# Kernel optimization log

Hardware: AMD Instinct MI355X
Metric: run time of the kernel (lower is better)

The kernel has to match this reference:

```python
import jax, jax.numpy as jnp
import numpy as np

B, L, F, DM, H, DFF, NL, PRED = 8, 1000, 7, 512, 8, 2048, 4, 50
DK = DM // H           # head dim 64
P = DK // 4            # learned-mask proj dim 16
EPS = 1e-5
SCALE = 1.0 / float(np.sqrt(DK))


def _ln(x, g, b):
    m = jnp.mean(x, -1, keepdims=True)
    v = jnp.mean((x - m) ** 2, -1, keepdims=True)
    return (x - m) / jnp.sqrt(v + EPS) * g + b


def _make_pe():
    pos = np.arange(L, dtype=np.float32)[:, None]
    div = np.exp(np.arange(0, DM, 2, dtype=np.float32) * (-np.log(10000.0) / DM))
    pe = np.zeros((L, DM), dtype=np.float32)
    pe[:, 0::2] = np.sin(pos * div)
    pe[:, 1::2] = np.cos(pos * div)
    return jnp.asarray(pe)


def setup_inputs() -> dict:
    key = jax.random.key(0)
    ks = iter(jax.random.split(key, 40))
    def w(shape, s=0.02):
        return jax.random.normal(next(ks), shape, jnp.float32) * s
    return {
        "x": jax.random.normal(next(ks), (B, L, F), jnp.float32),
        "emb_w": w((F, DM)), "emb_b": jnp.zeros((DM,), jnp.float32),
        "pe": _make_pe(),
        "Wq": w((NL, DM, DM)), "bq": jnp.zeros((NL, DM), jnp.float32),
        "Wk": w((NL, DM, DM)), "bk": jnp.zeros((NL, DM), jnp.float32),
        "Wv": w((NL, DM, DM)), "bv": jnp.zeros((NL, DM), jnp.float32),
        "Wo": w((NL, DM, DM)), "bo": jnp.zeros((NL, DM), jnp.float32),
        "W1": w((NL, DM, DFF)), "b1": jnp.zeros((NL, DFF), jnp.float32),
        "W2": w((NL, DFF, DM)), "b2": jnp.zeros((NL, DM), jnp.float32),
        "g1": jnp.ones((NL, DM), jnp.float32), "be1": jnp.zeros((NL, DM), jnp.float32),
        "g2": jnp.ones((NL, DM), jnp.float32), "be2": jnp.zeros((NL, DM), jnp.float32),
        "lm_qw": w((DK, P)), "lm_qb": jnp.zeros((P,), jnp.float32),
        "lm_kw": w((DK, P)), "lm_kb": jnp.zeros((P,), jnp.float32),
        "gn": jnp.ones((DM,), jnp.float32), "bn": jnp.zeros((DM,), jnp.float32),
        "fc_w": w((DM, PRED)), "fc_b": jnp.zeros((PRED,), jnp.float32),
    }


def reference(x, emb_w, emb_b, pe, Wq, bq, Wk, bk, Wv, bv, Wo, bo,
              W1, b1, W2, b2, g1, be1, g2, be2,
              lm_qw, lm_qb, lm_kw, lm_kb, gn, bn, fc_w, fc_b):
    # eval mode: dropout = identity
    h = x @ emb_w + emb_b + pe[None]                 # [B,L,DM]
    for i in range(NL):
        q = (h @ Wq[i] + bq[i]).reshape(B, L, H, DK)
        k = (h @ Wk[i] + bk[i]).reshape(B, L, H, DK)
        v = (h @ Wv[i] + bv[i]).reshape(B, L, H, DK)
        scores = jnp.einsum('blhd,bshd->bhls', q, k) * SCALE
        # shared LearnedMask: per-head Q/K projection to P dims, tanh bias
        qp = q @ lm_qw + lm_qb                       # [B,L,H,P]
        kp = k @ lm_kw + lm_kb                       # [B,S,H,P]
        scores = scores + jnp.tanh(jnp.einsum('blhp,bshp->bhls', qp, kp))
        attn = jax.nn.softmax(scores, axis=-1)       # mask_flag=False: no mask
        ctx = jnp.einsum('bhls,bshd->blhd', attn, v).reshape(B, L, DM)
        h = _ln(h + ctx @ Wo[i] + bo[i], g1[i], be1[i])
        y = jax.nn.relu(h @ W1[i] + b1[i]) @ W2[i] + b2[i]
        h2 = _ln(h + y, g2[i], be2[i])
        h = _ln(h2 + y, g2[i], be2[i])               # module applies norm2 twice
    h = _ln(h, gn, bn)                               # Encoder final norm
    return h[:, -1, :] @ fc_w + fc_b                 # [B, PRED]
```

## Files before the change

### kernel.cpp

```cpp
#include <hip/hip_runtime.h>
#include <math.h>

#define B_    8
#define L_    1000
#define F_    7
#define DM_   512
#define H_    8
#define DFF_  2048
#define NL_   4
#define PRED_ 50
#define DK_   64
#define P_    16
#define EPS_  1e-5f
#define QKVS  1536

#define L2E_   1.4426950408889634f
#define C_QS   0.18033688011112042f
#define WS_QP  16.0f
#define BS_QP  2.8853900817779268f
#define SHFT_  24.0f

typedef unsigned short u16;
typedef __bf16 bf16x8 __attribute__((ext_vector_type(8)));
typedef float  f32x4  __attribute__((ext_vector_type(4)));

__device__ inline float wave_reduce_sum(float x) {
#pragma unroll
  for (int off = 32; off >= 1; off >>= 1) x += __shfl_xor(x, off, 64);
  return x;
}
__device__ inline u16 f2bf(float f) {
  unsigned int u = __float_as_uint(f);
  unsigned int r = u + 0x7FFFu + ((u >> 16) & 1u);
  return (u16)(r >> 16);
}
__device__ inline float bf2f(u16 u) { return __uint_as_float(((unsigned int)u) << 16); }
__device__ inline float fexp2(float x) { return __builtin_amdgcn_exp2f(x); }
__device__ inline float frcp(float x) { return __builtin_amdgcn_rcpf(x); }

union bfrag { bf16x8 b; uint4 q; u16 u[8]; };

__device__ inline void gload16(const u16* g, u16* l) {
  __builtin_amdgcn_global_load_lds(
      (const __attribute__((address_space(1))) void*)g,
      (__attribute__((address_space(3))) void*)l, 16, 0, 0);
}

__global__ __launch_bounds__(256)
void transpose_w(const float* __restrict__ in, u16* __restrict__ out,
                 int K, int N, size_t in_lstride, size_t out_lstride,
                 int row_off, int out_ld) {
  __shared__ float tile[32][33];
  int z = blockIdx.z;
  int kk0 = blockIdx.y * 32, nn0 = blockIdx.x * 32;
  int tx = threadIdx.x & 31, ty = threadIdx.x >> 5;
  const float* ip = in + z * in_lstride;
  u16* op = out + z * out_lstride;
#pragma unroll
  for (int i = 0; i < 4; i++)
    tile[ty + i * 8][tx] = ip[(size_t)(kk0 + ty + i * 8) * N + nn0 + tx];
  __syncthreads();
#pragma unroll
  for (int i = 0; i < 4; i++)
    op[(size_t)(row_off + nn0 + ty + i * 8) * out_ld + kk0 + tx] = f2bf(tile[tx][ty + i * 8]);
}

__global__ __launch_bounds__(256)
void vtrans_kernel(const u16* __restrict__ qkv, u16* __restrict__ vtg) {
  __shared__ u16 tile[32][33];
  int bh = blockIdx.z;
  int b = bh >> 3, hh = bh & 7;
  int k0 = blockIdx.x * 32;
  int d0 = blockIdx.y * 32;
  int tx = threadIdx.x & 31, ty = threadIdx.x >> 5;
#pragma unroll
  for (int i = 0; i < 4; i++) {
    int key = k0 + ty + i * 8;
    u16 v = 0;
    if (key < L_) v = qkv[(size_t)(b * L_ + key) * QKVS + 1024 + hh * DK_ + d0 + tx];
    tile[ty + i * 8][tx] = v;
  }
  __syncthreads();
#pragma unroll
  for (int i = 0; i < 4; i++)
    vtg[((size_t)bh * DK_ + d0 + ty + i * 8) * 1024 + k0 + tx] = tile[tx][ty + i * 8];
}

__global__ __launch_bounds__(256)
void concat_bias(const float* __restrict__ bq, const float* __restrict__ bk,
                 const float* __restrict__ bv, float* __restrict__ bqkv) {
  int i = blockIdx.x * 256 + threadIdx.x;
  int l = i / QKVS, j = i % QKVS;
  float v = (j < 512) ? bq[l * 512 + j] : (j < 1024) ? bk[l * 512 + j - 512]
                                                     : bv[l * 512 + j - 1024];
  bqkv[i] = v;
}

__global__ __launch_bounds__(512)
void embed_kernel(const float* __restrict__ x, const float* __restrict__ emb_w,
                  const float* __restrict__ emb_b, const float* __restrict__ pe,
                  float* __restrict__ h, u16* __restrict__ h16) {
  int bl = blockIdx.x;
  int l = bl % L_;
  int d = threadIdx.x;
  const float* xr = x + (size_t)bl * F_;
  float acc = emb_b[d] + pe[(size_t)l * DM_ + d];
#pragma unroll
  for (int f = 0; f < F_; f++) acc = fmaf(xr[f], emb_w[f * DM_ + d], acc);
  h[(size_t)bl * DM_ + d] = acc;
  h16[(size_t)bl * DM_ + d] = f2bf(acc);
}

template<int BN>
__global__ __launch_bounds__(256)
void gemm16(const u16* __restrict__ A, const u16* __restrict__ Bt,
            const float* __restrict__ bias, const float* __restrict__ resid,
            float* __restrict__ C32, u16* __restrict__ C16,
            int M, int K, int N, int relu, int nscale, float sval) {
  constexpr int NTW = BN / 32;
  constexpr int BG  = BN / 32;
  __shared__ u16 As[128 * 64];
  __shared__ u16 Bs[BN * 64];
  int t = threadIdx.x;
  int w = t >> 6, lane = t & 63;
  int wr = w >> 1, wc = w & 1;
  int mloc = lane & 15, quad = lane >> 4;
  int m0 = blockIdx.y * 128, n0 = blockIdx.x * BN;

  const u16* agp[4]; u16* alds[4];
#pragma unroll
  for (int j = 0; j < 4; j++) {
    int r = w * 32 + j * 8 + (lane >> 3);
    int gm = m0 + r; if (gm > M - 1) gm = M - 1;
    int ch = (lane & 7) ^ (r & 7);
    agp[j] = A + (size_t)gm * K + ch * 8;
    alds[j] = As + (w * 32 + j * 8) * 64;
  }
  const u16* bgp[BG]; u16* blds[BG];
#pragma unroll
  for (int j = 0; j < BG; j++) {
    int r = w * (8 * BG) + j * 8 + (lane >> 3);
    int ch = (lane & 7) ^ (r & 7);
    bgp[j] = Bt + (size_t)(n0 + r) * K + ch * 8;
    blds[j] = Bs + (w * (8 * BG) + j * 8) * 64;
  }
  const u16* apt[2][4];
#pragma unroll
  for (int mi = 0; mi < 4; mi++) {
    int tr = wr * 64 + mi * 16 + mloc;
    apt[0][mi] = As + tr * 64 + ((quad ^ (tr & 7)) * 8);
    apt[1][mi] = As + tr * 64 + (((4 + quad) ^ (tr & 7)) * 8);
  }
  const u16* bpt[2][NTW];
#pragma unroll
  for (int nt = 0; nt < NTW; nt++) {
    int tr = wc * (BN / 2) + nt * 16 + mloc;
    bpt[0][nt] = Bs + tr * 64 + ((quad ^ (tr & 7)) * 8);
    bpt[1][nt] = Bs + tr * 64 + (((4 + quad) ^ (tr & 7)) * 8);
  }

  f32x4 acc[4][NTW];
#pragma unroll
  for (int mi = 0; mi < 4; mi++)
#pragma unroll
    for (int nt = 0; nt < NTW; nt++) acc[mi][nt] = (f32x4){0.f, 0.f, 0.f, 0.f};

  for (int k0 = 0; k0 < K; k0 += 64) {
    __syncthreads();
    #pragma unroll
    for (int j = 0; j < 4; j++) gload16(agp[j] + k0, alds[j]);
    #pragma unroll
    for (int j = 0; j < BG; j++) gload16(bgp[j] + k0, blds[j]);
    __syncthreads();
#pragma unroll
    for (int kc = 0; kc < 2; kc++) {
      bf16x8 af[4], bv[NTW];
#pragma unroll
      for (int mi = 0; mi < 4; mi++) af[mi] = *(const bf16x8*)apt[kc][mi];
#pragma unroll
      for (int nt = 0; nt < NTW; nt++) bv[nt] = *(const bf16x8*)bpt[kc][nt];
#pragma unroll
      for (int mi = 0; mi < 4; mi++)
#pragma unroll
        for (int nt = 0; nt < NTW; nt++)
          acc[mi][nt] = __builtin_amdgcn_mfma_f32_16x16x32_bf16(af[mi], bv[nt], acc[mi][nt], 0, 0, 0);
    }
  }

#pragma unroll
  for (int mi = 0; mi < 4; mi++) {
#pragma unroll
    for (int r = 0; r < 4; r++) {
      int m = m0 + wr * 64 + mi * 16 + quad * 4 + r;
      if (m >= M) continue;
      size_t crow = (size_t)m * N;
#pragma unroll
      for (int nt = 0; nt < NTW; nt++) {
        int n = n0 + wc * (BN / 2) + nt * 16 + mloc;
        float vsum = acc[mi][nt][r] + bias[n];
        if (resid) vsum += resid[crow + n];
        if (n < nscale) vsum *= sval;
        if (relu) vsum = fmaxf(vsum, 0.f);
        if (C32) C32[crow + n] = vsum;
        if (C16) C16[crow + n] = f2bf(vsum);
      }
    }
  }
}

__global__ __launch_bounds__(128)
void lmproj_kernel(const u16* __restrict__ qkv,
                   const float* __restrict__ wq, const float* __restrict__ bq,
                   const float* __restrict__ wk, const float* __restrict__ bk,
                   u16* __restrict__ qp, u16* __restrict__ kp) {
  int bl = blockIdx.x;
  int which = blockIdx.y;
  int t = threadIdx.x;
  int hh = t >> 4, p = t & 15;
  const float* w  = which ? wk : wq;
  const float* bb = which ? bk : bq;
  u16* dst        = which ? kp : qp;
  float wscale = which ? 1.0f : WS_QP;
  float bscale = which ? 1.0f : BS_QP;
  const u16* s = qkv + (size_t)bl * QKVS + (which ? 512 : 0) + hh * DK_;
  float acc = 0.f;
#pragma unroll
  for (int d = 0; d < DK_; d++) acc = fmaf(bf2f(s[d]), w[d * P_ + p], acc);
  dst[((size_t)bl * H_ + hh) * P_ + p] = f2bf(fmaf(acc, wscale, bb[p] * bscale));
}

#define KT   128
#define LDP  136
#define KPLD 24
__global__ __launch_bounds__(256)
void attn_mfma_kernel(const u16* __restrict__ qkv, const u16* __restrict__ qpg,
                      const u16* __restrict__ kpg, const u16* __restrict__ vtg,
                      u16* __restrict__ ctx) {
  __shared__ u16 KsPs[4 * 16 * LDP];
  __shared__ u16 Vt[64 * KT];
  __shared__ u16 Kp[KT * KPLD];

  int Lid = blockIdx.x;
  int qt = Lid >> 6;
  int bh = ((Lid & 7) << 3) | ((Lid >> 3) & 7);
  int b = bh >> 3, hh = bh & 7;
  int l0 = qt * 64;
  int t = threadIdx.x;
  int wv = t >> 6, lane = t & 63;
  int m = lane & 15, quad = lane >> 4;

  int lq = l0 + wv * 16 + m; if (lq > L_ - 1) lq = L_ - 1;
  const u16* qrow = qkv + (size_t)(b * L_ + lq) * QKVS + hh * DK_;
  bf16x8 qa0 = *(const bf16x8*)(qrow + quad * 8);
  bf16x8 qa1 = *(const bf16x8*)(qrow + 32 + quad * 8);
  bfrag qpa;
  if (quad < 2) {
    qpa.q = *(const uint4*)(qpg + ((size_t)(b * L_ + lq) * H_ + hh) * P_ + quad * 8);
  } else {
    qpa.q = make_uint4(0u, 0u, 0u, 0u);
  }

  const u16* ks_g = qkv + ((size_t)b * L_ + (t >> 3)) * QKVS + 512 + hh * DK_
                    + ((t & 7) ^ ((t >> 3) & 7)) * 8;
  u16* ks_l = KsPs + (t >> 6) * 512;
  const u16* vt_g = vtg + ((size_t)bh * DK_ + (t >> 4)) * 1024
                    + (((t & 15) ^ (t >> 4)) * 8);
  u16* vt_l = Vt + (t >> 6) * 512;

  f32x4 O[4];
#pragma unroll
  for (int nt = 0; nt < 4; nt++) O[nt] = (f32x4){0.f, 0.f, 0.f, 0.f};
  float lrun[4] = {0.f, 0.f, 0.f, 0.f};

  u16* pw = KsPs + wv * (16 * LDP);
  const u16* pr0 = pw + m * LDP + quad * 8;

  for (int s0 = 0; s0 < L_; s0 += KT) {
    uint4 p0, p1;
    if (t < KT) {
      int sg2 = s0 + t; if (sg2 > L_ - 1) sg2 = L_ - 1;
      const u16* pr = kpg + ((size_t)(b * L_ + sg2) * H_ + hh) * P_;
      p0 = *(const uint4*)(pr);
      p1 = *(const uint4*)(pr + 8);
    }
    __syncthreads();
#pragma unroll
    for (int j = 0; j < 4; j++) {
      gload16(ks_g + ((size_t)s0 + j * 32) * QKVS, ks_l + j * 2048);
      gload16(vt_g + s0 + (size_t)j * 16 * 1024, vt_l + j * 2048);
    }
    if (t < KT) {
      *(uint4*)&Kp[t * KPLD]     = p0;
      *(uint4*)&Kp[t * KPLD + 8] = p1;
    }
    __syncthreads();

    float scp[8][4];
    const f32x4 zz = (f32x4){0.f, 0.f, 0.f, 0.f};
#pragma unroll
    for (int nt = 0; nt < 8; nt++) {
      const u16* kb = KsPs + (nt * 16 + m) * 64;
      int x0 = ((quad) ^ (m & 7)) * 8;
      int x1 = ((4 + quad) ^ (m & 7)) * 8;
      f32x4 sacc = __builtin_amdgcn_mfma_f32_16x16x32_bf16(qa0, *(const bf16x8*)(kb + x0), zz, 0, 0, 0);
      sacc = __builtin_amdgcn_mfma_f32_16x16x32_bf16(qa1, *(const bf16x8*)(kb + x1), sacc, 0, 0, 0);
      bf16x8 kpf = *(const bf16x8*)(Kp + (nt * 16 + m) * KPLD + (quad & 1) * 8);
      f32x4 macc = __builtin_amdgcn_mfma_f32_16x16x32_bf16(qpa.b, kpf, zz, 0, 0, 0);
#pragma unroll
      for (int r = 0; r < 4; r++) {
        float e = fexp2(macc[r]);
        float d = frcp(e + 1.f);
        float th = fmaf(d, -2.f * L2E_, L2E_);
        scp[nt][r] = sacc[r] + th;
      }
    }
    if (s0 + KT > L_) {
#pragma unroll
      for (int nt = 0; nt < 8; nt++) {
        if (s0 + nt * 16 + m >= L_) {
#pragma unroll
          for (int r = 0; r < 4; r++) scp[nt][r] = -3e38f;
        }
      }
    }
#pragma unroll
    for (int nt = 0; nt < 8; nt++)
#pragma unroll
      for (int r = 0; r < 4; r++) {
        float p = fexp2(scp[nt][r] - SHFT_);
        scp[nt][r] = p;
        lrun[r] += p;
      }

    __syncthreads();

#pragma unroll
    for (int nt = 0; nt < 8; nt++)
#pragma unroll
      for (int r = 0; r < 4; r++)
        pw[(quad * 4 + r) * LDP + nt * 16 + m] = f2bf(scp[nt][r]);

#pragma unroll
    for (int kc = 0; kc < 4; kc++) {
      bf16x8 pa = *(const bf16x8*)(pr0 + kc * 32);
#pragma unroll
      for (int nt = 0; nt < 4; nt++) {
        const u16* vb = Vt + (nt * 16 + m) * KT + (((kc * 4 + quad) ^ m) * 8);
        O[nt] = __builtin_amdgcn_mfma_f32_16x16x32_bf16(pa, *(const bf16x8*)vb, O[nt], 0, 0, 0);
      }
    }
  }

  float inv[4];
#pragma unroll
  for (int r = 0; r < 4; r++) {
#pragma unroll
    for (int msk = 1; msk < 16; msk <<= 1) lrun[r] += __shfl_xor(lrun[r], msk, 64);
    inv[r] = frcp(lrun[r]);
  }
#pragma unroll
  for (int r = 0; r < 4; r++) {
    int l = l0 + wv * 16 + quad * 4 + r;
    if (l >= L_) continue;
    u16* crow = ctx + ((size_t)(b * L_ + l)) * DM_ + hh * DK_;
#pragma unroll
    for (int nt = 0; nt < 4; nt++) crow[nt * 16 + m] = f2bf(O[nt][r] * inv[r]);
  }
}

__global__ __launch_bounds__(256)
void ln_kernel(const float* __restrict__ a, const float* __restrict__ badd,
               const float* __restrict__ g, const float* __restrict__ be,
               float* __restrict__ o, u16* __restrict__ o16) {
  int row = blockIdx.x;
  int t = threadIdx.x;
  size_t base = (size_t)row * DM_;
  float x0 = a[base + t], x1 = a[base + t + 256];
  if (badd) { x0 += badd[base + t]; x1 += badd[base + t + 256]; }
  float s = wave_reduce_sum(x0 + x1);
  float ss = wave_reduce_sum(x0 * x0 + x1 * x1);
  __shared__ float sh_s[4], sh_ss[4];
  int wv = t >> 6, lane = t & 63;
  if (lane == 0) { sh_s[wv] = s; sh_ss[wv] = ss; }
  __syncthreads();
  float S = sh_s[0] + sh_s[1] + sh_s[2] + sh_s[3];
  float SS = sh_ss[0] + sh_ss[1] + sh_ss[2] + sh_ss[3];
  float mean = S * (1.0f / DM_);
  float var = SS * (1.0f / DM_) - mean * mean;
  float rstd = rsqrtf(var + EPS_);
  float r0 = (x0 - mean) * rstd * g[t] + be[t];
  float r1 = (x1 - mean) * rstd * g[t + 256] + be[t + 256];
  o[base + t] = r0; o[base + t + 256] = r1;
  if (o16) { o16[base + t] = f2bf(r0); o16[base + t + 256] = f2bf(r1); }
}

__global__ __launch_bounds__(256)
void ln2x_kernel(const float* __restrict__ hin, const float* __restrict__ y,
                 const float* __restrict__ g, const float* __restrict__ be,
                 float* __restrict__ o32, u16* __restrict__ o16) {
  int row = blockIdx.x;
  int t = threadIdx.x;
  size_t base = (size_t)row * DM_;
  float y0 = y[base + t], y1 = y[base + t + 256];
  float x0 = hin[base + t] + y0, x1 = hin[base + t + 256] + y1;
  __shared__ float sh_s[4], sh_ss[4];
  int wv = t >> 6, lane = t & 63;
  float g0 = g[t], g1v = g[t + 256], b0 = be[t], b1v = be[t + 256];

  float s = wave_reduce_sum(x0 + x1);
  float ss = wave_reduce_sum(x0 * x0 + x1 * x1);
  if (lane == 0) { sh_s[wv] = s; sh_ss[wv] = ss; }
  __syncthreads();
  float S = sh_s[0] + sh_s[1] + sh_s[2] + sh_s[3];
  float SS = sh_ss[0] + sh_ss[1] + sh_ss[2] + sh_ss[3];
  float mean = S * (1.0f / DM_);
  float var = SS * (1.0f / DM_) - mean * mean;
  float rstd = rsqrtf(var + EPS_);
  float h20 = (x0 - mean) * rstd * g0 + b0 + y0;
  float h21 = (x1 - mean) * rstd * g1v + b1v + y1;
  __syncthreads();

  s = wave_reduce_sum(h20 + h21);
  ss = wave_reduce_sum(h20 * h20 + h21 * h21);
  if (lane == 0) { sh_s[wv] = s; sh_ss[wv] = ss; }
  __syncthreads();
  S = sh_s[0] + sh_s[1] + sh_s[2] + sh_s[3];
  SS = sh_ss[0] + sh_ss[1] + sh_ss[2] + sh_ss[3];
  mean = S * (1.0f / DM_);
  var = SS * (1.0f / DM_) - mean * mean;
  rstd = rsqrtf(var + EPS_);
  float r0 = (h20 - mean) * rstd * g0 + b0;
  float r1 = (h21 - mean) * rstd * g1v + b1v;
  o32[base + t] = r0; o32[base + t + 256] = r1;
  if (o16) { o16[base + t] = f2bf(r0); o16[base + t + 256] = f2bf(r1); }
}

__global__ __launch_bounds__(512)
void final_kernel(const float* __restrict__ h, const float* __restrict__ gn,
                  const float* __restrict__ bn, const float* __restrict__ fcw,
                  const float* __restrict__ fcb, float* __restrict__ out) {
  int b = blockIdx.x;
  int t = threadIdx.x;
  size_t base = ((size_t)b * L_ + (L_ - 1)) * DM_;
  float x = h[base + t];
  float s = wave_reduce_sum(x);
  float ss = wave_reduce_sum(x * x);
  __shared__ float sh_s[8], sh_ss[8];
  int wv = t >> 6, lane = t & 63;
  if (lane == 0) { sh_s[wv] = s; sh_ss[wv] = ss; }
  __syncthreads();
  float S = 0.f, SS = 0.f;
#pragma unroll
  for (int i = 0; i < 8; i++) { S += sh_s[i]; SS += sh_ss[i]; }
  float mean = S * (1.0f / DM_);
  float var = SS * (1.0f / DM_) - mean * mean;
  float rstd = rsqrtf(var + EPS_);
  __shared__ float hn[DM_];
  hn[t] = (x - mean) * rstd * gn[t] + bn[t];
  __syncthreads();
  if (t < PRED_) {
    float acc = fcb[t];
#pragma unroll 8
    for (int d = 0; d < DM_; d++) acc = fmaf(hn[d], fcw[d * PRED_ + t], acc);
    out[b * PRED_ + t] = acc;
  }
}

extern "C" void kernel_launch(void* const* d_in, const int* in_sizes, int n_in,
                              void* d_out, int out_size, void* d_ws, size_t ws_size,
                              hipStream_t stream) {
  const float* x     = (const float*)d_in[0];
  const float* emb_w = (const float*)d_in[1];
  const float* emb_b = (const float*)d_in[2];
  const float* pe    = (const float*)d_in[3];
  const float* Wq = (const float*)d_in[4];  const float* bq = (const float*)d_in[5];
  const float* Wk = (const float*)d_in[6];  const float* bk = (const float*)d_in[7];
  const float* Wv = (const float*)d_in[8];  const float* bv = (const float*)d_in[9];
  const float* Wo = (const float*)d_in[10]; const float* bo = (const float*)d_in[11];
  const float* W1 = (const float*)d_in[12]; const float* b1 = (const float*)d_in[13];
  const float* W2 = (const float*)d_in[14]; const float* b2 = (const float*)d_in[15];
  const float* g1 = (const float*)d_in[16]; const float* be1 = (const float*)d_in[17];
  const float* g2 = (const float*)d_in[18]; const float* be2 = (const float*)d_in[19];
  const float* lm_qw = (const float*)d_in[20]; const float* lm_qb = (const float*)d_in[21];
  const float* lm_kw = (const float*)d_in[22]; const float* lm_kb = (const float*)d_in[23];
  const float* gn = (const float*)d_in[24]; const float* bn = (const float*)d_in[25];
  const float* fc_w = (const float*)d_in[26]; const float* fc_b = (const float*)d_in[27];
  float* out = (float*)d_out;

  const size_t ROWS = (size_t)B_ * L_;
  u16* qkv16 = (u16*)d_ws;
  u16* ctx16 = qkv16 + ROWS * QKVS;
  u16* ffn1  = qkv16;
  u16* h16   = ctx16 + ROWS * DM_;
  u16* qp16  = h16 + ROWS * DM_;
  u16* kp16  = qp16 + ROWS * H_ * P_;
  u16* Wqkv_t = kp16 + ROWS * H_ * P_;
  u16* Wo_t   = Wqkv_t + (size_t)NL_ * QKVS * DM_;
  u16* W1_t   = Wo_t + (size_t)NL_ * DM_ * DM_;
  u16* W2_t   = W1_t + (size_t)NL_ * DFF_ * DM_;
  float* h32  = (float*)(W2_t + (size_t)NL_ * DM_ * DFF_);
  float* t0   = h32 + ROWS * DM_;
  float* bqkv = t0 + ROWS * DM_;
  u16* vtg    = (u16*)t0;

  transpose_w<<<dim3(16, 16, NL_), 256, 0, stream>>>(Wq, Wqkv_t, DM_, DM_, (size_t)DM_ * DM_, (size_t)QKVS * DM_, 0, DM_);
  transpose_w<<<dim3(16, 16, NL_), 256, 0, stream>>>(Wk, Wqkv_t, DM_, DM_, (size_t)DM_ * DM_, (size_t)QKVS * DM_, 512, DM_);
  transpose_w<<<dim3(16, 16, NL_), 256, 0, stream>>>(Wv, Wqkv_t, DM_, DM_, (size_t)DM_ * DM_, (size_t)QKVS * DM_, 1024, DM_);
  transpose_w<<<dim3(16, 16, NL_), 256, 0, stream>>>(Wo, Wo_t, DM_, DM_, (size_t)DM_ * DM_, (size_t)DM_ * DM_, 0, DM_);
  transpose_w<<<dim3(64, 16, NL_), 256, 0, stream>>>(W1, W1_t, DM_, DFF_, (size_t)DM_ * DFF_, (size_t)DFF_ * DM_, 0, DM_);
  transpose_w<<<dim3(16, 64, NL_), 256, 0, stream>>>(W2, W2_t, DFF_, DM_, (size_t)DFF_ * DM_, (size_t)DM_ * DFF_, 0, DFF_);
  concat_bias<<<NL_ * QKVS / 256, 256, 0, stream>>>(bq, bk, bv, bqkv);

  embed_kernel<<<dim3((unsigned)ROWS), 512, 0, stream>>>(x, emb_w, emb_b, pe, h32, h16);

  dim3 g_qkv(QKVS / 128, 63);
  dim3 g_ffn1(DFF_ / 128, 63);
  dim3 g_n512(DM_ / 64, 63);
  dim3 g_attn(1024);
  dim3 g_lm((unsigned)ROWS, 2);

  for (int i = 0; i < NL_; i++) {
    gemm16<128><<<g_qkv, 256, 0, stream>>>(h16, Wqkv_t + (size_t)i * QKVS * DM_,
        bqkv + i * QKVS, nullptr, nullptr, qkv16, 8000, DM_, QKVS, 0, 512, C_QS);

    lmproj_kernel<<<g_lm, 128, 0, stream>>>(qkv16, lm_qw, lm_qb, lm_kw, lm_kb, qp16, kp16);
    vtrans_kernel<<<dim3(32, 2, B_ * H_), 256, 0, stream>>>(qkv16, vtg);

    attn_mfma_kernel<<<g_attn, 256, 0, stream>>>(qkv16, qp16, kp16, vtg, ctx16);

    gemm16<64><<<g_n512, 256, 0, stream>>>(ctx16, Wo_t + (size_t)i * DM_ * DM_,
        bo + i * DM_, h32, t0, nullptr, 8000, DM_, DM_, 0, 0, 1.0f);
    ln_kernel<<<dim3((unsigned)ROWS), 256, 0, stream>>>(t0, nullptr, g1 + i * DM_, be1 + i * DM_, h32, h16);

    gemm16<128><<<g_ffn1, 256, 0, stream>>>(h16, W1_t + (size_t)i * DFF_ * DM_,
        b1 + i * DFF_, nullptr, nullptr, ffn1, 8000, DM_, DFF_, 1, 0, 1.0f);
    gemm16<64><<<g_n512, 256, 0, stream>>>(ffn1, W2_t + (size_t)i * DM_ * DFF_,
        b2 + i * DM_, nullptr, t0, nullptr, 8000, DFF_, DM_, 0, 0, 1.0f);

    ln2x_kernel<<<dim3((unsigned)ROWS), 256, 0, stream>>>(h32, t0, g2 + i * DM_, be2 + i * DM_, h32, h16);
  }

  final_kernel<<<B_, 512, 0, stream>>>(h32, gn, bn, fc_w, fc_b, out);
}
```

Baseline: 1.260 ms.

## Fold learned-mask projections into QKV GEMM and write transposed V from epilogue

Precomputes fused weights (Wq·lm_qw, Wk·lm_kw) and biases so the QKV GEMM also emits the 16-dim mask projections as extra output columns (N grows from 1536 to 1792). This removes the separate lmproj kernel. The GEMM epilogue also writes V straight into the transposed per-head layout, replacing vtrans_kernel with a small kernel that only zeroes the padding. The attention kernel is reworked to compute scores and P chunk by chunk, with a smaller P buffer, which removes a barrier and the large score register array. In exchange the GEMM does more work, and the mask projection now sees different bf16 rounding because it is applied to weights rather than to bf16 Q/K.

```diff
diff --git a/kernel.cpp b/kernel.cpp
--- a/kernel.cpp
+++ b/kernel.cpp
@@ -12,11 +12,10 @@
 #define DK_   64
 #define P_    16
 #define EPS_  1e-5f
-#define QKVS  1536
+#define QKVS  1792
 
 #define L2E_   1.4426950408889634f
 #define C_QS   0.18033688011112042f
-#define WS_QP  16.0f
 #define BS_QP  2.8853900817779268f
 #define SHFT_  24.0f
 
@@ -66,33 +65,63 @@
 }
 
 __global__ __launch_bounds__(256)
-void vtrans_kernel(const u16* __restrict__ qkv, u16* __restrict__ vtg) {
-  __shared__ u16 tile[32][33];
-  int bh = blockIdx.z;
-  int b = bh >> 3, hh = bh & 7;
-  int k0 = blockIdx.x * 32;
-  int d0 = blockIdx.y * 32;
-  int tx = threadIdx.x & 31, ty = threadIdx.x >> 5;
-#pragma unroll
-  for (int i = 0; i < 4; i++) {
-    int key = k0 + ty + i * 8;
-    u16 v = 0;
-    if (key < L_) v = qkv[(size_t)(b * L_ + key) * QKVS + 1024 + hh * DK_ + d0 + tx];
-    tile[ty + i * 8][tx] = v;
-  }
-  __syncthreads();
-#pragma unroll
-  for (int i = 0; i < 4; i++)
-    vtg[((size_t)bh * DK_ + d0 + ty + i * 8) * 1024 + k0 + tx] = tile[tx][ty + i * 8];
+void wfuse_kernel(const float* __restrict__ Wq, const float* __restrict__ Wk,
+                  const float* __restrict__ lmqw, const float* __restrict__ lmkw,
+                  u16* __restrict__ Wt) {
+  int hh = blockIdx.x, side = blockIdx.y, layer = blockIdx.z;
+  const float* W = (side ? Wk : Wq) + (size_t)layer * 512 * 512;
+  const float* lw = side ? lmkw : lmqw;
+  float scale = side ? 1.0f : BS_QP;
+  __shared__ float lws[64][17];
+  int t = threadIdx.x;
+  for (int i = t; i < 1024; i += 256) lws[i >> 4][i & 15] = lw[i];
+  __syncthreads();
+  int p = t & 15, kk = t >> 4;
+  u16* orow = Wt + (size_t)layer * QKVS * 512 + (size_t)(1536 + side * 128 + hh * 16 + p) * 512;
+  for (int kb = 0; kb < 32; kb++) {
+    int k = kb * 16 + kk;
+    const float* wr = W + (size_t)k * 512 + hh * 64;
+    float acc = 0.f;
+#pragma unroll
+    for (int d = 0; d < 64; d++) acc = fmaf(wr[d], lws[d][p], acc);
+    orow[k] = f2bf(acc * scale);
+  }
+}
+
+__global__ __launch_bounds__(192)
+void vzero_kernel(u16* __restrict__ vtg) {
+  int bh = blockIdx.x;
+  int t = threadIdx.x;
+  int dk = t / 3, c = t - dk * 3;
+  *(uint4*)(vtg + ((size_t)bh * 64 + dk) * 1024 + 1000 + c * 8) =
+      make_uint4(0u, 0u, 0u, 0u);
 }
 
 __global__ __launch_bounds__(256)
 void concat_bias(const float* __restrict__ bq, const float* __restrict__ bk,
-                 const float* __restrict__ bv, float* __restrict__ bqkv) {
+                 const float* __restrict__ bv,
+                 const float* __restrict__ lmqw, const float* __restrict__ lmqb,
+                 const float* __restrict__ lmkw, const float* __restrict__ lmkb,
+                 float* __restrict__ bqkv) {
   int i = blockIdx.x * 256 + threadIdx.x;
   int l = i / QKVS, j = i % QKVS;
-  float v = (j < 512) ? bq[l * 512 + j] : (j < 1024) ? bk[l * 512 + j - 512]
-                                                     : bv[l * 512 + j - 1024];
+  float v;
+  if (j < 512) v = bq[l * 512 + j];
+  else if (j < 1024) v = bk[l * 512 + j - 512];
+  else if (j < 1536) v = bv[l * 512 + j - 1024];
+  else if (j < 1664) {
+    int hh = (j - 1536) >> 4, p = (j - 1536) & 15;
+    float acc = lmqb[p];
+#pragma unroll
+    for (int d = 0; d < 64; d++) acc = fmaf(bq[l * 512 + hh * 64 + d], lmqw[d * 16 + p], acc);
+    v = acc * BS_QP;
+  } else {
+    int hh = (j - 1664) >> 4, p = (j - 1664) & 15;
+    float acc = lmkb[p];
+#pragma unroll
+    for (int d = 0; d < 64; d++) acc = fmaf(bk[l * 512 + hh * 64 + d], lmkw[d * 16 + p], acc);
+    v = acc;
+  }
   bqkv[i] = v;
 }
 
@@ -115,7 +144,7 @@
 __global__ __launch_bounds__(256)
 void gemm16(const u16* __restrict__ A, const u16* __restrict__ Bt,
             const float* __restrict__ bias, const float* __restrict__ resid,
-            float* __restrict__ C32, u16* __restrict__ C16,
+            float* __restrict__ C32, u16* __restrict__ C16, u16* __restrict__ vtg,
             int M, int K, int N, int relu, int nscale, float sval) {
   constexpr int NTW = BN / 32;
   constexpr int BG  = BN / 32;
@@ -167,9 +196,9 @@
 
   for (int k0 = 0; k0 < K; k0 += 64) {
     __syncthreads();
-    #pragma unroll
+#pragma unroll
     for (int j = 0; j < 4; j++) gload16(agp[j] + k0, alds[j]);
-    #pragma unroll
+#pragma unroll
     for (int j = 0; j < BG; j++) gload16(bgp[j] + k0, blds[j]);
     __syncthreads();
 #pragma unroll
@@ -189,56 +218,52 @@
 
 #pragma unroll
   for (int mi = 0; mi < 4; mi++) {
-#pragma unroll
-    for (int r = 0; r < 4; r++) {
-      int m = m0 + wr * 64 + mi * 16 + quad * 4 + r;
-      if (m >= M) continue;
-      size_t crow = (size_t)m * N;
-#pragma unroll
-      for (int nt = 0; nt < NTW; nt++) {
-        int n = n0 + wc * (BN / 2) + nt * 16 + mloc;
-        float vsum = acc[mi][nt][r] + bias[n];
-        if (resid) vsum += resid[crow + n];
-        if (n < nscale) vsum *= sval;
-        if (relu) vsum = fmaxf(vsum, 0.f);
-        if (C32) C32[crow + n] = vsum;
-        if (C16) C16[crow + n] = f2bf(vsum);
+    int m_r0 = m0 + wr * 64 + mi * 16 + quad * 4;
+#pragma unroll
+    for (int nt = 0; nt < NTW; nt++) {
+      int nbase = n0 + wc * (BN / 2) + nt * 16;
+      int n = nbase + mloc;
+      if (vtg && nbase >= 1024 && nbase < 1536) {
+        if (m_r0 < M) {
+          int bb = (m_r0 * 67109) >> 26;
+          int ll = m_r0 - bb * 1000;
+          int hh2 = (n - 1024) >> 6, dk = n & 63;
+          float bn_ = bias[n];
+          union { uint2 d; u16 s[4]; } pk;
+#pragma unroll
+          for (int r = 0; r < 4; r++) pk.s[r] = f2bf(acc[mi][nt][r] + bn_);
+          u16* dst = vtg + ((size_t)(bb * 8 + hh2) * 64 + dk) * 1024 + ll;
+          *(uint2*)dst = pk.d;
+        }
+      } else {
+        float bn_ = bias[n];
+#pragma unroll
+        for (int r = 0; r < 4; r++) {
+          int m = m_r0 + r;
+          if (m >= M) continue;
+          size_t crow = (size_t)m * N;
+          float vsum = acc[mi][nt][r] + bn_;
+          if (resid) vsum += resid[crow + n];
+          if (n < nscale) vsum *= sval;
+          if (relu) vsum = fmaxf(vsum, 0.f);
+          if (C32) C32[crow + n] = vsum;
+          if (C16) C16[crow + n] = f2bf(vsum);
+        }
       }
     }
   }
 }
 
-__global__ __launch_bounds__(128)
-void lmproj_kernel(const u16* __restrict__ qkv,
-                   const float* __restrict__ wq, const float* __restrict__ bq,
-                   const float* __restrict__ wk, const float* __restrict__ bk,
-                   u16* __restrict__ qp, u16* __restrict__ kp) {
-  int bl = blockIdx.x;
-  int which = blockIdx.y;
-  int t = threadIdx.x;
-  int hh = t >> 4, p = t & 15;
-  const float* w  = which ? wk : wq;
-  const float* bb = which ? bk : bq;
-  u16* dst        = which ? kp : qp;
-  float wscale = which ? 1.0f : WS_QP;
-  float bscale = which ? 1.0f : BS_QP;
-  const u16* s = qkv + (size_t)bl * QKVS + (which ? 512 : 0) + hh * DK_;
-  float acc = 0.f;
-#pragma unroll
-  for (int d = 0; d < DK_; d++) acc = fmaf(bf2f(s[d]), w[d * P_ + p], acc);
-  dst[((size_t)bl * H_ + hh) * P_ + p] = f2bf(fmaf(acc, wscale, bb[p] * bscale));
-}
-
 #define KT   128
-#define LDP  136
 #define KPLD 24
-__global__ __launch_bounds__(256)
-void attn_mfma_kernel(const u16* __restrict__ qkv, const u16* __restrict__ qpg,
-                      const u16* __restrict__ kpg, const u16* __restrict__ vtg,
+#define PSLD 40
+__global__ __launch_bounds__(256)
+void attn_mfma_kernel(const u16* __restrict__ qkv, const u16* __restrict__ vtg,
                       u16* __restrict__ ctx) {
-  __shared__ u16 KsPs[4 * 16 * LDP];
+  __shared__ u16 Ks[KT * 64];
   __shared__ u16 Vt[64 * KT];
   __shared__ u16 Kp[KT * KPLD];
+  __shared__ u16 Ps[4 * 16 * PSLD];
 
   int Lid = blockIdx.x;
   int qt = Lid >> 6;
@@ -255,14 +280,14 @@
   bf16x8 qa1 = *(const bf16x8*)(qrow + 32 + quad * 8);
   bfrag qpa;
   if (quad < 2) {
-    qpa.q = *(const uint4*)(qpg + ((size_t)(b * L_ + lq) * H_ + hh) * P_ + quad * 8);
+    qpa.q = *(const uint4*)(qkv + (size_t)(b * L_ + lq) * QKVS + 1536 + hh * P_ + quad * 8);
   } else {
     qpa.q = make_uint4(0u, 0u, 0u, 0u);
   }
 
   const u16* ks_g = qkv + ((size_t)b * L_ + (t >> 3)) * QKVS + 512 + hh * DK_
                     + ((t & 7) ^ ((t >> 3) & 7)) * 8;
-  u16* ks_l = KsPs + (t >> 6) * 512;
+  u16* ks_l = Ks + (t >> 6) * 512;
   const u16* vt_g = vtg + ((size_t)bh * DK_ + (t >> 4)) * 1024
                     + (((t & 15) ^ (t >> 4)) * 8);
   u16* vt_l = Vt + (t >> 6) * 512;
@@ -272,14 +297,15 @@
   for (int nt = 0; nt < 4; nt++) O[nt] = (f32x4){0.f, 0.f, 0.f, 0.f};
   float lrun[4] = {0.f, 0.f, 0.f, 0.f};
 
-  u16* pw = KsPs + wv * (16 * LDP);
-  const u16* pr0 = pw + m * LDP + quad * 8;
+  u16* pw = Ps + wv * (16 * PSLD);
+  const u16* pr0 = pw + m * PSLD + quad * 8;
+  const f32x4 zz = (f32x4){0.f, 0.f, 0.f, 0.f};
 
   for (int s0 = 0; s0 < L_; s0 += KT) {
     uint4 p0, p1;
     if (t < KT) {
       int sg2 = s0 + t; if (sg2 > L_ - 1) sg2 = L_ - 1;
-      const u16* pr = kpg + ((size_t)(b * L_ + sg2) * H_ + hh) * P_;
+      const u16* pr = qkv + (size_t)(b * L_ + sg2) * QKVS + 1664 + hh * P_;
       p0 = *(const uint4*)(pr);
       p1 = *(const uint4*)(pr + 8);
     }
@@ -295,58 +321,42 @@
     }
     __syncthreads();
 
-    float scp[8][4];
-    const f32x4 zz = (f32x4){0.f, 0.f, 0.f, 0.f};
-#pragma unroll
-    for (int nt = 0; nt < 8; nt++) {
-      const u16* kb = KsPs + (nt * 16 + m) * 64;
-      int x0 = ((quad) ^ (m & 7)) * 8;
-      int x1 = ((4 + quad) ^ (m & 7)) * 8;
-      f32x4 sacc = __builtin_amdgcn_mfma_f32_16x16x32_bf16(qa0, *(const bf16x8*)(kb + x0), zz, 0, 0, 0);
-      sacc = __builtin_amdgcn_mfma_f32_16x16x32_bf16(qa1, *(const bf16x8*)(kb + x1), sacc, 0, 0, 0);
-      bf16x8 kpf = *(const bf16x8*)(Kp + (nt * 16 + m) * KPLD + (quad & 1) * 8);
-      f32x4 macc = __builtin_amdgcn_mfma_f32_16x16x32_bf16(qpa.b, kpf, zz, 0, 0, 0);
-#pragma unroll
-      for (int r = 0; r < 4; r++) {
-        float e = fexp2(macc[r]);
-        float d = frcp(e + 1.f);
-        float th = fmaf(d, -2.f * L2E_, L2E_);
-        scp[nt][r] = sacc[r] + th;
-      }
-    }
-    if (s0 + KT > L_) {
-#pragma unroll
-      for (int nt = 0; nt < 8; nt++) {
-        if (s0 + nt * 16 + m >= L_) {
-#pragma unroll
-          for (int r = 0; r < 4; r++) scp[nt][r] = -3e38f;
+#pragma unroll
+    for (int kc = 0; kc < 4; kc++) {
+      float pv2[2][4];
+#pragma unroll
+      for (int h2 = 0; h2 < 2; h2++) {
+        int nt = kc * 2 + h2;
+        const u16* kb = Ks + (nt * 16 + m) * 64;
+        int x0 = ((quad) ^ (m & 7)) * 8;
+        int x1 = ((4 + quad) ^ (m & 7)) * 8;
+        f32x4 sacc = __builtin_amdgcn_mfma_f32_16x16x32_bf16(qa0, *(const bf16x8*)(kb + x0), zz, 0, 0, 0);
+        sacc = __builtin_amdgcn_mfma_f32_16x16x32_bf16(qa1, *(const bf16x8*)(kb + x1), sacc, 0, 0, 0);
+        bf16x8 kpf = *(const bf16x8*)(Kp + (nt * 16 + m) * KPLD + (quad & 1) * 8);
+        f32x4 macc = __builtin_amdgcn_mfma_f32_16x16x32_bf16(qpa.b, kpf, zz, 0, 0, 0);
+        bool oob = (s0 + nt * 16 + m) >= L_;
+#pragma unroll
+        for (int r = 0; r < 4; r++) {
+          float e = fexp2(macc[r]);
+          float d = frcp(e + 1.f);
+          float th = fmaf(d, -2.f * L2E_, L2E_);
+          float s = sacc[r] + th;
+          if (oob) s = -3e38f;
+          float p = fexp2(s - SHFT_);
+          pv2[h2][r] = p;
+          lrun[r] += p;
         }
       }
-    }
-#pragma unroll
-    for (int nt = 0; nt < 8; nt++)
-#pragma unroll
-      for (int r = 0; r < 4; r++) {
-        float p = fexp2(scp[nt][r] - SHFT_);
-        scp[nt][r] = p;
-        lrun[r] += p;
-      }
-
-    __syncthreads();
-
-#pragma unroll
-    for (int nt = 0; nt < 8; nt++)
-#pragma unroll
-      for (int r = 0; r < 4; r++)
-        pw[(quad * 4 + r) * LDP + nt * 16 + m] = f2bf(scp[nt][r]);
-
-#pragma unroll
-    for (int kc = 0; kc < 4; kc++) {
-      bf16x8 pa = *(const bf16x8*)(pr0 + kc * 32);
-#pragma unroll
-      for (int nt = 0; nt < 4; nt++) {
-        const u16* vb = Vt + (nt * 16 + m) * KT + (((kc * 4 + quad) ^ m) * 8);
-        O[nt] = __builtin_amdgcn_mfma_f32_16x16x32_bf16(pa, *(const bf16x8*)vb, O[nt], 0, 0, 0);
+#pragma unroll
+      for (int h2 = 0; h2 < 2; h2++)
+#pragma unroll
+        for (int r = 0; r < 4; r++)
+          pw[(quad * 4 + r) * PSLD + h2 * 16 + m] = f2bf(pv2[h2][r]);
+      bf16x8 pa = *(const bf16x8*)pr0;
+#pragma unroll
+      for (int ntd = 0; ntd < 4; ntd++) {
+        const u16* vb = Vt + (ntd * 16 + m) * KT + (((kc * 4 + quad) ^ m) * 8);
+        O[ntd] = __builtin_amdgcn_mfma_f32_16x16x32_bf16(pa, *(const bf16x8*)vb, O[ntd], 0, 0, 0);
       }
     }
   }
@@ -492,9 +502,7 @@
   u16* ctx16 = qkv16 + ROWS * QKVS;
   u16* ffn1  = qkv16;
   u16* h16   = ctx16 + ROWS * DM_;
-  u16* qp16  = h16 + ROWS * DM_;
-  u16* kp16  = qp16 + ROWS * H_ * P_;
-  u16* Wqkv_t = kp16 + ROWS * H_ * P_;
+  u16* Wqkv_t = h16 + ROWS * DM_;
   u16* Wo_t   = Wqkv_t + (size_t)NL_ * QKVS * DM_;
   u16* W1_t   = Wo_t + (size_t)NL_ * DM_ * DM_;
   u16* W2_t   = W1_t + (size_t)NL_ * DFF_ * DM_;
@@ -509,7 +517,8 @@
   transpose_w<<<dim3(16, 16, NL_), 256, 0, stream>>>(Wo, Wo_t, DM_, DM_, (size_t)DM_ * DM_, (size_t)DM_ * DM_, 0, DM_);
   transpose_w<<<dim3(64, 16, NL_), 256, 0, stream>>>(W1, W1_t, DM_, DFF_, (size_t)DM_ * DFF_, (size_t)DFF_ * DM_, 0, DM_);
   transpose_w<<<dim3(16, 64, NL_), 256, 0, stream>>>(W2, W2_t, DFF_, DM_, (size_t)DFF_ * DM_, (size_t)DM_ * DFF_, 0, DFF_);
-  concat_bias<<<NL_ * QKVS / 256, 256, 0, stream>>>(bq, bk, bv, bqkv);
+  wfuse_kernel<<<dim3(H_, 2, NL_), 256, 0, stream>>>(Wq, Wk, lm_qw, lm_kw, Wqkv_t);
+  concat_bias<<<NL_ * QKVS / 256, 256, 0, stream>>>(bq, bk, bv, lm_qw, lm_qb, lm_kw, lm_kb, bqkv);
 
   embed_kernel<<<dim3((unsigned)ROWS), 512, 0, stream>>>(x, emb_w, emb_b, pe, h32, h16);
 
@@ -517,25 +526,23 @@
   dim3 g_ffn1(DFF_ / 128, 63);
   dim3 g_n512(DM_ / 64, 63);
   dim3 g_attn(1024);
-  dim3 g_lm((unsigned)ROWS, 2);
 
   for (int i = 0; i < NL_; i++) {
     gemm16<128><<<g_qkv, 256, 0, stream>>>(h16, Wqkv_t + (size_t)i * QKVS * DM_,
-        bqkv + i * QKVS, nullptr, nullptr, qkv16, 8000, DM_, QKVS, 0, 512, C_QS);
-
-    lmproj_kernel<<<g_lm, 128, 0, stream>>>(qkv16, lm_qw, lm_qb, lm_kw, lm_kb, qp16, kp16);
-    vtrans_kernel<<<dim3(32, 2, B_ * H_), 256, 0, stream>>>(qkv16, vtg);
-
-    attn_mfma_kernel<<<g_attn, 256, 0, stream>>>(qkv16, qp16, kp16, vtg, ctx16);
+        bqkv + i * QKVS, nullptr, nullptr, qkv16, vtg, 8000, DM_, QKVS, 0, 512, C_QS);
+
+    vzero_kernel<<<64, 192, 0, stream>>>(vtg);
+
+    attn_mfma_kernel<<<g_attn, 256, 0, stream>>>(qkv16, vtg, ctx16);
 
     gemm16<64><<<g_n512, 256, 0, stream>>>(ctx16, Wo_t + (size_t)i * DM_ * DM_,
-        bo + i * DM_, h32, t0, nullptr, 8000, DM_, DM_, 0, 0, 1.0f);
+        bo + i * DM_, h32, t0, nullptr, nullptr, 8000, DM_, DM_, 0, 0, 1.0f);
     ln_kernel<<<dim3((unsigned)ROWS), 256, 0, stream>>>(t0, nullptr, g1 + i * DM_, be1 + i * DM_, h32, h16);
 
     gemm16<128><<<g_ffn1, 256, 0, stream>>>(h16, W1_t + (size_t)i * DFF_ * DM_,
-        b1 + i * DFF_, nullptr, nullptr, ffn1, 8000, DM_, DFF_, 1, 0, 1.0f);
+        b1 + i * DFF_, nullptr, nullptr, ffn1, nullptr, 8000, DM_, DFF_, 1, 0, 1.0f);
     gemm16<64><<<g_n512, 256, 0, stream>>>(ffn1, W2_t + (size_t)i * DM_ * DFF_,
-        b2 + i * DM_, nullptr, t0, nullptr, 8000, DFF_, DM_, 0, 0, 1.0f);
+        b2 + i * DM_, nullptr, t0, nullptr, nullptr, 8000, DFF_, DM_, 0, 0, 1.0f);
 
     ln2x_kernel<<<dim3((unsigned)ROWS), 256, 0, stream>>>(h32, t0, g2 + i * DM_, be2 + i * DM_, h32, h16);
   }
```

Measured after the change: 1.223 ms. 1.03x faster.
